# Optimization experiments

Measured on AMD Instinct MI355X. Metric: run time of the kernel, lower is better.

Reference implementation:

```python
import jax, jax.numpy as jnp
import numpy as np

B, DX, DY, H, T, L = 256, 256, 256, 512, 128, 2
EPS = 1e-5


def setup_inputs() -> dict:
    key = jax.random.key(0)
    ks = jax.random.split(key, 16)
    s = 0.02
    return {
        "inputx": jax.random.normal(ks[0], (B, DX, T), dtype=jnp.float32),
        "inputy": jax.random.normal(ks[1], (B, DY, T), dtype=jnp.float32),
        # stacked gate weights: f,i,o for T-path and F-path, [L, 3H, Dx+Dy+H]
        "WTg": jax.random.normal(ks[2], (L, 3 * H, DX + DY + H), dtype=jnp.float32) * s,
        "bTg": jax.random.normal(ks[3], (L, 3 * H), dtype=jnp.float32) * s,
        "WFg": jax.random.normal(ks[4], (L, 3 * H, DX + DY + H), dtype=jnp.float32) * s,
        "bFg": jax.random.normal(ks[5], (L, 3 * H), dtype=jnp.float32) * s,
        # candidate cell weights
        "WTc": jax.random.normal(ks[6], (L, H, DX + H), dtype=jnp.float32) * s,
        "bTc": jax.random.normal(ks[7], (L, H), dtype=jnp.float32) * s,
        "WFc": jax.random.normal(ks[8], (L, H, DY + H), dtype=jnp.float32) * s,
        "bFc": jax.random.normal(ks[9], (L, H), dtype=jnp.float32) * s,
        # batchnorm affine params per layer
        "gammaT": jnp.ones((L, H), dtype=jnp.float32),
        "betaT": jnp.zeros((L, H), dtype=jnp.float32),
        "gammaF": jnp.ones((L, H), dtype=jnp.float32),
        "betaF": jnp.zeros((L, H), dtype=jnp.float32),
    }


def _batchnorm(h, gamma, beta):
    # train-mode BN over batch dim, biased variance (torch semantics)
    mu = jnp.mean(h, axis=0, keepdims=True)
    var = jnp.mean((h - mu) ** 2, axis=0, keepdims=True)
    return (h - mu) * jax.lax.rsqrt(var + EPS) * gamma + beta


def _forward(inputx, inputy, WTg, bTg, WFg, bFg, WTc, bTc, WFc, bFc,
             gammaT, betaT, gammaF, betaF):
    nL = WTg.shape[0]
    b, h = inputx.shape[0], gammaT.shape[1]
    zeros = jnp.zeros((nL, b, h), dtype=inputx.dtype)

    def step(carry, xy):
        hT, hF, CT, CF = carry  # each [L, B, H]
        x, y = xy  # [B, Dx], [B, Dy]
        hT_n, hF_n, CT_n, CF_n = [], [], [], []
        for i in range(nL):
            catT = jnp.concatenate([x, y, hT[i]], axis=1)
            catF = jnp.concatenate([x, y, hF[i]], axis=1)
            gT = jax.nn.sigmoid(catT @ WTg[i].T + bTg[i])  # [B, 3H]
            gF = jax.nn.sigmoid(catF @ WFg[i].T + bFg[i])
            fT, iT, oT = jnp.split(gT, 3, axis=1)
            fF, iF, oF = jnp.split(gF, 3, axis=1)
            cT = jnp.tanh(jnp.concatenate([x, hT[i]], axis=1) @ WTc[i].T + bTc[i])
            cF = jnp.tanh(jnp.concatenate([y, hF[i]], axis=1) @ WFc[i].T + bFc[i])
            CTi = fT * CT[i] + iT * cT
            CFi = fF * CF[i] + iF * cF
            hTi = oT * jnp.tanh(CTi)
            hFi = oF * jnp.tanh(CFi)
            hT_n.append(hTi); hF_n.append(hFi); CT_n.append(CTi); CF_n.append(CFi)
        hT = jnp.stack(hT_n); hF = jnp.stack(hF_n)
        CT = jnp.stack(CT_n); CF = jnp.stack(CF_n)
        # output comes from last layer only; BN in train mode
        outT = _batchnorm(hT[-1], gammaT[-1], betaT[-1])
        outF = _batchnorm(hF[-1], gammaF[-1], betaF[-1])
        return (hT, hF, CT, CF), (outT, outF)

    xs = (jnp.transpose(inputx, (2, 0, 1)), jnp.transpose(inputy, (2, 0, 1)))
    _, (outT_seq, outF_seq) = jax.lax.scan(step, (zeros, zeros, zeros, zeros), xs)
    # [T, B, H] -> [B, H, T] (torch.stack(..., dim=2))
    return jnp.transpose(outT_seq, (1, 2, 0)), jnp.transpose(outF_seq, (1, 2, 0))


def reference(inputx, inputy, WTg, bTg, WFg, bFg, WTc, bTc, WFc, bFc,
              gammaT, betaT, gammaF, betaF):
    return _forward(inputx, inputy, WTg, bTg, WFg, bFg, WTc, bTc, WFc, bFc,
                    gammaT, betaT, gammaF, betaF)
```

## Files before the change

### kernel.cpp

```cpp
#include <hip/hip_runtime.h>

#define NBLK 256
#define NTHR 512

typedef __attribute__((ext_vector_type(8))) short s16x8;
typedef __attribute__((ext_vector_type(8))) __bf16 bf16x8;
typedef __attribute__((ext_vector_type(4))) float f32x4;

__device__ __forceinline__ ushort f2bf(float f) {
  uint u = __float_as_uint(f);
  return (ushort)((u + 0x7FFFu + ((u >> 16) & 1u)) >> 16);
}
__device__ __forceinline__ float bf2f(ushort s) {
  return __uint_as_float(((uint)s) << 16);
}
__device__ __forceinline__ float sigm(float x) { return 1.f / (1.f + __expf(-x)); }
__device__ __forceinline__ float tanhf_(float x) {
  x = fminf(9.f, fmaxf(-9.f, x));
  float e = __expf(2.f * x);
  return (e - 1.f) / (e + 1.f);
}

__global__ void init_k(uint* __restrict__ bar) {
  int i = blockIdx.x * blockDim.x + threadIdx.x;
  if (i < 512) bar[i] = 0u;
}

__global__ void xyt_k(const float* __restrict__ x, const float* __restrict__ y,
                      ushort* __restrict__ xyT) {
  __shared__ ushort sT[64 * 130];
  const int bid = blockIdx.x;
  const int chunk = bid & 7;
  const int b = bid >> 3;
  const int d0 = (chunk & 3) * 64;
  const float* src = ((chunk < 4) ? x : y) + ((size_t)b * 256 + d0) * 128;
  const int tid = threadIdx.x;
  const int tt = tid & 127, rr = tid >> 7;
#pragma unroll
  for (int i = 0; i < 32; ++i) {
    int row = i * 2 + rr;
    sT[row * 130 + tt] = f2bf(src[(size_t)row * 128 + tt]);
  }
  __syncthreads();
  const int dbase = ((chunk < 4) ? 0 : 256) + d0;
#pragma unroll
  for (int i = 0; i < 16; ++i) {
    int idx = tid + i * 256;
    int t = idx >> 5, j = idx & 31;
    uint v = (uint)sT[(2 * j) * 130 + t] | ((uint)sT[(2 * j + 1) * 130 + t] << 16);
    *(uint*)(xyT + ((size_t)t * 256 + b) * 512 + dbase + 2 * j) = v;
  }
}

__launch_bounds__(NTHR, 2)
__global__ void seq_k(const ushort* __restrict__ xyT,
                      ushort* __restrict__ hist,
                      const float* __restrict__ WTg, const float* __restrict__ WFg,
                      const float* __restrict__ WTc, const float* __restrict__ WFc,
                      const float* __restrict__ bTg, const float* __restrict__ bFg,
                      const float* __restrict__ bTc, const float* __restrict__ bFc,
                      uint* bar) {
  extern __shared__ char smem[];
  float* sAcc = (float*)(smem + 98304);

  const int tid = threadIdx.x;
  const int bid = blockIdx.x;
  const int mt = bid & 7;
  const int cg = (bid >> 3) & 15;
  const int s = bid >> 7;
  const int g = s * 8 + mt;
  const int m0 = mt * 32;
  const int j0 = cg * 32;
  const int w = tid >> 6;
  const int l = tid & 63;
  const int l15 = l & 15;
  const int q16 = (l >> 4) * 16;
  const bool isGate = (w < 6);
  uint* fl = bar + (g << 4);

  s16x8 wreg[32];
  if (isGate) {
    const int gt = w >> 1, half = w & 1;
    const float* Wp = ((s == 0) ? WTg : WFg) + 1572864
                    + ((size_t)(gt * 512 + j0 + half * 16 + l15)) * 1024 + (q16 >> 1);
#pragma unroll
    for (int kk = 0; kk < 32; ++kk) {
      s16x8 v;
#pragma unroll
      for (int e = 0; e < 8; ++e) v[e] = (short)f2bf(Wp[kk * 32 + e]);
      wreg[kk] = v;
    }
  } else {
    const int half = w & 1;
    const float* Wp = ((s == 0) ? WTc : WFc) + 393216
                    + ((size_t)(j0 + half * 16 + l15)) * 768 + (q16 >> 1);
#pragma unroll
    for (int kk = 0; kk < 24; ++kk) {
      s16x8 v;
#pragma unroll
      for (int e = 0; e < 8; ++e) v[e] = (short)f2bf(Wp[kk * 32 + e]);
      wreg[kk] = v;
    }
  }

  const int ro = tid >> 4;
  const int cc0 = (tid & 15) * 2;
  const int ehalf = cc0 >> 4;
  const int ec16 = cc0 & 15;
  float bfv0, bfv1, biv0, biv1, bov0, bov1, bcv0, bcv1;
  {
    const float* bg = ((s == 0) ? bTg : bFg) + 1536;
    const float* bc = ((s == 0) ? bTc : bFc) + 512;
    int col = j0 + cc0;
    bfv0 = bg[col];        bfv1 = bg[col + 1];
    biv0 = bg[512 + col];  biv1 = bg[513 + col];
    bov0 = bg[1024 + col]; bov1 = bg[1025 + col];
    bcv0 = bc[col];        bcv1 = bc[col + 1];
  }
  float C0 = 0.f, C1 = 0.f;

  auto stage_row = [&](const ushort* gbase, char* lbase, int r) {
    const char* srow = (const char*)(gbase + (size_t)r * 512);
    int off = (l * 16) ^ ((r & 7) << 4);
    __builtin_amdgcn_global_load_lds(
        (const __attribute__((address_space(1))) void*)(srow + off),
        (__attribute__((address_space(3))) void*)(lbase + (r << 10)), 16, 0, 0);
  };
  auto stage_row_coh = [&](const ushort* gbase, char* lbase, int r) {
    const char* srow = (const char*)(gbase + (size_t)r * 512);
    int off = (l * 16) ^ ((r & 7) << 4);
    __builtin_amdgcn_global_load_lds(
        (const __attribute__((address_space(1))) void*)(srow + off),
        (__attribute__((address_space(3))) void*)(lbase + (r << 10)), 16, 0, 17);
  };

  {
#pragma unroll
    for (int i = 0; i < 4; ++i) stage_row(xyT + (size_t)m0 * 512, smem, (w << 2) + i);
  }
  __syncthreads();

  const int sw = (l15 & 7) << 4;
  for (int t = 0; t < 128; ++t) {
    const int cur = t & 1;
    char* xyb = smem + cur * 32768;
    char* xybn = smem + (cur ^ 1) * 32768;
    char* hb = smem + 65536;

    f32x4 acc0 = {0.f, 0.f, 0.f, 0.f};
    f32x4 acc1 = {0.f, 0.f, 0.f, 0.f};

    {
      const char* base0 = xyb + (l15 << 10);
      const char* base1 = xyb + ((16 + l15) << 10);
      if (isGate) {
#pragma unroll
        for (int kk = 0; kk < 16; ++kk) {
          int c2 = (kk * 64 + q16) ^ sw;
          s16x8 a0 = *(const s16x8*)(base0 + c2);
          s16x8 a1 = *(const s16x8*)(base1 + c2);
          acc0 = __builtin_amdgcn_mfma_f32_16x16x32_bf16(
              __builtin_bit_cast(bf16x8, a0), __builtin_bit_cast(bf16x8, wreg[kk]), acc0, 0, 0, 0);
          acc1 = __builtin_amdgcn_mfma_f32_16x16x32_bf16(
              __builtin_bit_cast(bf16x8, a1), __builtin_bit_cast(bf16x8, wreg[kk]), acc1, 0, 0, 0);
        }
      } else {
#pragma unroll
        for (int kk = 0; kk < 8; ++kk) {
          int c2 = ((s * 512 + kk * 64 + q16)) ^ sw;
          s16x8 a0 = *(const s16x8*)(base0 + c2);
          s16x8 a1 = *(const s16x8*)(base1 + c2);
          acc0 = __builtin_amdgcn_mfma_f32_16x16x32_bf16(
              __builtin_bit_cast(bf16x8, a0), __builtin_bit_cast(bf16x8, wreg[kk]), acc0, 0, 0, 0);
          acc1 = __builtin_amdgcn_mfma_f32_16x16x32_bf16(
              __builtin_bit_cast(bf16x8, a1), __builtin_bit_cast(bf16x8, wreg[kk]), acc1, 0, 0, 0);
        }
      }
    }

    if (w == 0 && t) {
      const uint tgt = (uint)t;
      while (true) {
        uint v = (l < 16)
                     ? __hip_atomic_load(fl + l, __ATOMIC_RELAXED, __HIP_MEMORY_SCOPE_SYSTEM)
                     : tgt;
        if (__all((int)(v >= tgt))) break;
        __builtin_amdgcn_s_sleep(1);
      }
    }
    __builtin_amdgcn_s_barrier();

    if (t) {
      const ushort* hsrc = hist + (((size_t)s * 128 + (t - 1)) * 256 + m0) * 512;
#pragma unroll
      for (int i = 0; i < 4; ++i) stage_row_coh(hsrc, hb, (w << 2) + i);
    }
    {
      const int tn = (t < 127) ? t + 1 : 127;
      const ushort* xyNext = xyT + ((size_t)(tn * 256 + m0)) * 512;
#pragma unroll
      for (int i = 0; i < 4; ++i) stage_row(xyNext, xybn, (w << 2) + i);
    }

    asm volatile("s_waitcnt vmcnt(4)" ::: "memory");
    __builtin_amdgcn_sched_barrier(0);
    __builtin_amdgcn_s_barrier();
    __builtin_amdgcn_sched_barrier(0);

    if (t) {
      const char* base0 = hb + (l15 << 10);
      const char* base1 = hb + ((16 + l15) << 10);
      if (isGate) {
#pragma unroll
        for (int kk = 0; kk < 16; ++kk) {
          int c2 = (kk * 64 + q16) ^ sw;
          s16x8 a0 = *(const s16x8*)(base0 + c2);
          s16x8 a1 = *(const s16x8*)(base1 + c2);
          acc0 = __builtin_amdgcn_mfma_f32_16x16x32_bf16(
              __builtin_bit_cast(bf16x8, a0), __builtin_bit_cast(bf16x8, wreg[16 + kk]), acc0, 0, 0, 0);
          acc1 = __builtin_amdgcn_mfma_f32_16x16x32_bf16(
              __builtin_bit_cast(bf16x8, a1), __builtin_bit_cast(bf16x8, wreg[16 + kk]), acc1, 0, 0, 0);
        }
      } else {
#pragma unroll
        for (int kk = 0; kk < 16; ++kk) {
          int c2 = (kk * 64 + q16) ^ sw;
          s16x8 a0 = *(const s16x8*)(base0 + c2);
          s16x8 a1 = *(const s16x8*)(base1 + c2);
          acc0 = __builtin_amdgcn_mfma_f32_16x16x32_bf16(
              __builtin_bit_cast(bf16x8, a0), __builtin_bit_cast(bf16x8, wreg[8 + kk]), acc0, 0, 0, 0);
          acc1 = __builtin_amdgcn_mfma_f32_16x16x32_bf16(
              __builtin_bit_cast(bf16x8, a1), __builtin_bit_cast(bf16x8, wreg[8 + kk]), acc1, 0, 0, 0);
        }
      }
    }

#pragma unroll
    for (int rg = 0; rg < 4; ++rg) {
      sAcc[w * 576 + ((q16 >> 2) + rg) * 18 + l15] = acc0[rg];
      sAcc[w * 576 + (16 + (q16 >> 2) + rg) * 18 + l15] = acc1[rg];
    }
    asm volatile("s_waitcnt lgkmcnt(0)" ::: "memory");
    __builtin_amdgcn_sched_barrier(0);
    __builtin_amdgcn_s_barrier();
    __builtin_amdgcn_sched_barrier(0);

    {
      const float2 pf = *(const float2*)&sAcc[(0 + ehalf) * 576 + ro * 18 + ec16];
      const float2 pi = *(const float2*)&sAcc[(2 + ehalf) * 576 + ro * 18 + ec16];
      const float2 po = *(const float2*)&sAcc[(4 + ehalf) * 576 + ro * 18 + ec16];
      const float2 pc = *(const float2*)&sAcc[(6 + ehalf) * 576 + ro * 18 + ec16];
      float f0 = sigm(pf.x + bfv0), f1 = sigm(pf.y + bfv1);
      float i0 = sigm(pi.x + biv0), i1 = sigm(pi.y + biv1);
      float o0 = sigm(po.x + bov0), o1 = sigm(po.y + bov1);
      float c0 = tanhf_(pc.x + bcv0), c1 = tanhf_(pc.y + bcv1);
      C0 = f0 * C0 + i0 * c0;
      C1 = f1 * C1 + i1 * c1;
      float h0 = o0 * tanhf_(C0);
      float h1 = o1 * tanhf_(C1);
      uint hp = (uint)f2bf(h0) | (((uint)f2bf(h1)) << 16);
      __hip_atomic_store(
          (uint*)(hist + (((size_t)s * 128 + t) * 256 + m0 + ro) * 512 + j0 + cc0), hp,
          __ATOMIC_RELAXED, __HIP_MEMORY_SCOPE_SYSTEM);
    }
    __syncthreads();
    if (tid == 0)
      __hip_atomic_store(fl + cg, (uint)(t + 1), __ATOMIC_RELAXED, __HIP_MEMORY_SCOPE_SYSTEM);
  }
}

__global__ void bnstat_k(const ushort* __restrict__ hist,
                         const float* __restrict__ gT, const float* __restrict__ beT,
                         const float* __restrict__ gF, const float* __restrict__ beF,
                         float* __restrict__ scale, float* __restrict__ shift) {
  const int t = blockIdx.x >> 1, s = blockIdx.x & 1;
  const int tid = threadIdx.x;
  const ushort* hp = hist + ((size_t)s * 128 + t) * 256 * 512;
  const float* gp = (s ? gF : gT) + 512;
  const float* bp = (s ? beF : beT) + 512;
#pragma unroll
  for (int hh = 0; hh < 2; ++hh) {
    const int h = tid + hh * 256;
    float sum = 0.f, sq = 0.f;
#pragma unroll 8
    for (int b = 0; b < 256; ++b) {
      float v = bf2f(hp[(size_t)b * 512 + h]);
      sum += v;
      sq += v * v;
    }
    float mu = sum * 0.00390625f;
    float var = sq * 0.00390625f - mu * mu;
    float sc = (1.0f / sqrtf(var + 1e-5f)) * gp[h];
    size_t o = ((size_t)s * 128 + t) * 512 + h;
    scale[o] = sc;
    shift[o] = bp[h] - mu * sc;
  }
}

__global__ void bnwrite_k(const ushort* __restrict__ hist, const float* __restrict__ scale,
                          const float* __restrict__ shift, float* __restrict__ out) {
  __shared__ float sT[64 * 129];
  const int bid = blockIdx.x;
  const int hc = bid & 7, b = (bid >> 3) & 255, s = bid >> 11;
  const int h0 = hc * 64;
  const int tid = threadIdx.x;
  const int hh = tid & 63, tq = tid >> 6;
#pragma unroll 4
  for (int tc = 0; tc < 32; ++tc) {
    const int t = tc * 4 + tq;
    const size_t so = ((size_t)s * 128 + t) * 512 + h0 + hh;
    float v = bf2f(hist[(((size_t)s * 128 + t) * 256 + b) * 512 + h0 + hh]);
    sT[hh * 129 + t] = v * scale[so] + shift[so];
  }
  __syncthreads();
  const int t2 = tid & 127, hq = tid >> 7;
#pragma unroll 4
  for (int i = 0; i < 32; ++i) {
    const int h = i * 2 + hq;
    out[(size_t)s * 16777216 + ((size_t)b * 512 + h0 + h) * 128 + t2] = sT[h * 129 + t2];
  }
}

extern "C" void kernel_launch(void* const* d_in, const int* in_sizes, int n_in,
                              void* d_out, int out_size, void* d_ws, size_t ws_size,
                              hipStream_t stream) {
  const float* inputx = (const float*)d_in[0];
  const float* inputy = (const float*)d_in[1];
  const float* WTg = (const float*)d_in[2];
  const float* bTg = (const float*)d_in[3];
  const float* WFg = (const float*)d_in[4];
  const float* bFg = (const float*)d_in[5];
  const float* WTc = (const float*)d_in[6];
  const float* bTc = (const float*)d_in[7];
  const float* WFc = (const float*)d_in[8];
  const float* bFc = (const float*)d_in[9];
  const float* gT = (const float*)d_in[10];
  const float* beT = (const float*)d_in[11];
  const float* gF = (const float*)d_in[12];
  const float* beF = (const float*)d_in[13];
  float* out = (float*)d_out;

  char* ws = (char*)d_ws;
  ushort* xyT = (ushort*)ws;
  ushort* hist = (ushort*)(ws + 34603008);
  float* scale = (float*)(ws + 101711872);
  float* shift = (float*)(ws + 102236160);
  uint* bar = (uint*)(ws + 102760448);

  init_k<<<2, 256, 0, stream>>>(bar);
  xyt_k<<<2048, 256, 0, stream>>>(inputx, inputy, xyT);

  hipFuncSetAttribute((const void*)seq_k, hipFuncAttributeMaxDynamicSharedMemorySize, 116736);
  void* args[11];
  args[0] = &xyT; args[1] = &hist;
  args[2] = &WTg; args[3] = &WFg; args[4] = &WTc; args[5] = &WFc;
  args[6] = &bTg; args[7] = &bFg; args[8] = &bTc; args[9] = &bFc;
  args[10] = &bar;
  hipLaunchCooperativeKernel((const void*)seq_k, dim3(NBLK), dim3(NTHR), args, 116736, stream);

  bnstat_k<<<256, 256, 0, stream>>>(hist, gT, beT, gF, beF, scale, shift);
  bnwrite_k<<<4096, 256, 0, stream>>>(hist, scale, shift, out);
}
```

Before: 611.6 us.

## Split wave work along K instead of N to reuse A fragments across two MFMA tiles

Each wave now covers both 16-column halves of its gate and half of the K range, rather than one column half over the full K range. Every A fragment read from LDS feeds two MFMAs, which halves the LDS read traffic per MFMA. The two K-partial sums are written to a wider shared accumulator and added during the elementwise gate stage. This adds LDS capacity for the accumulators, four accumulators per wave, and an extra add per gate element.

```diff
diff --git a/kernel.cpp b/kernel.cpp
--- a/kernel.cpp
+++ b/kernel.cpp
@@ -20,6 +20,9 @@
   float e = __expf(2.f * x);
   return (e - 1.f) / (e + 1.f);
 }
+
+#define MFMA(a, b, c) __builtin_amdgcn_mfma_f32_16x16x32_bf16( \
+    __builtin_bit_cast(bf16x8, a), __builtin_bit_cast(bf16x8, b), c, 0, 0, 0)
 
 __global__ void init_k(uint* __restrict__ bar) {
   int i = blockIdx.x * blockDim.x + threadIdx.x;
@@ -76,37 +79,55 @@
   const int l15 = l & 15;
   const int q16 = (l >> 4) * 16;
   const bool isGate = (w < 6);
+  const int kh = w & 1;
   uint* fl = bar + (g << 4);
 
-  s16x8 wreg[32];
+  s16x8 wreg[2][16];
   if (isGate) {
-    const int gt = w >> 1, half = w & 1;
-    const float* Wp = ((s == 0) ? WTg : WFg) + 1572864
-                    + ((size_t)(gt * 512 + j0 + half * 16 + l15)) * 1024 + (q16 >> 1);
-#pragma unroll
-    for (int kk = 0; kk < 32; ++kk) {
-      s16x8 v;
-#pragma unroll
-      for (int e = 0; e < 8; ++e) v[e] = (short)f2bf(Wp[kk * 32 + e]);
-      wreg[kk] = v;
+    const int gt = w >> 1;
+#pragma unroll
+    for (int p = 0; p < 2; ++p) {
+      const float* Wrow = ((s == 0) ? WTg : WFg) + 1572864
+                        + ((size_t)(gt * 512 + j0 + p * 16 + l15)) * 1024 + (q16 >> 1);
+#pragma unroll
+      for (int kk = 0; kk < 8; ++kk) {
+        s16x8 v;
+#pragma unroll
+        for (int e = 0; e < 8; ++e) v[e] = (short)f2bf(Wrow[kh * 256 + kk * 32 + e]);
+        wreg[p][kk] = v;
+      }
+#pragma unroll
+      for (int kk = 0; kk < 8; ++kk) {
+        s16x8 v;
+#pragma unroll
+        for (int e = 0; e < 8; ++e) v[e] = (short)f2bf(Wrow[512 + kh * 256 + kk * 32 + e]);
+        wreg[p][8 + kk] = v;
+      }
     }
   } else {
-    const int half = w & 1;
-    const float* Wp = ((s == 0) ? WTc : WFc) + 393216
-                    + ((size_t)(j0 + half * 16 + l15)) * 768 + (q16 >> 1);
-#pragma unroll
-    for (int kk = 0; kk < 24; ++kk) {
-      s16x8 v;
-#pragma unroll
-      for (int e = 0; e < 8; ++e) v[e] = (short)f2bf(Wp[kk * 32 + e]);
-      wreg[kk] = v;
+#pragma unroll
+    for (int p = 0; p < 2; ++p) {
+      const float* Wrow = ((s == 0) ? WTc : WFc) + 393216
+                        + ((size_t)(j0 + p * 16 + l15)) * 768 + (q16 >> 1);
+#pragma unroll
+      for (int kk = 0; kk < 4; ++kk) {
+        s16x8 v;
+#pragma unroll
+        for (int e = 0; e < 8; ++e) v[e] = (short)f2bf(Wrow[kh * 128 + kk * 32 + e]);
+        wreg[p][kk] = v;
+      }
+#pragma unroll
+      for (int kk = 0; kk < 8; ++kk) {
+        s16x8 v;
+#pragma unroll
+        for (int e = 0; e < 8; ++e) v[e] = (short)f2bf(Wrow[256 + kh * 256 + kk * 32 + e]);
+        wreg[p][4 + kk] = v;
+      }
     }
   }
 
   const int ro = tid >> 4;
   const int cc0 = (tid & 15) * 2;
-  const int ehalf = cc0 >> 4;
-  const int ec16 = cc0 & 15;
   float bfv0, bfv1, biv0, biv1, bov0, bov1, bcv0, bcv1;
   {
     const float* bg = ((s == 0) ? bTg : bFg) + 1536;
@@ -147,33 +168,35 @@
     char* xybn = smem + (cur ^ 1) * 32768;
     char* hb = smem + 65536;
 
-    f32x4 acc0 = {0.f, 0.f, 0.f, 0.f};
-    f32x4 acc1 = {0.f, 0.f, 0.f, 0.f};
+    f32x4 acc00 = {0.f, 0.f, 0.f, 0.f};
+    f32x4 acc01 = {0.f, 0.f, 0.f, 0.f};
+    f32x4 acc10 = {0.f, 0.f, 0.f, 0.f};
+    f32x4 acc11 = {0.f, 0.f, 0.f, 0.f};
 
     {
       const char* base0 = xyb + (l15 << 10);
       const char* base1 = xyb + ((16 + l15) << 10);
       if (isGate) {
 #pragma unroll
-        for (int kk = 0; kk < 16; ++kk) {
-          int c2 = (kk * 64 + q16) ^ sw;
+        for (int kk = 0; kk < 8; ++kk) {
+          int c2 = (kh * 512 + kk * 64 + q16) ^ sw;
           s16x8 a0 = *(const s16x8*)(base0 + c2);
           s16x8 a1 = *(const s16x8*)(base1 + c2);
-          acc0 = __builtin_amdgcn_mfma_f32_16x16x32_bf16(
-              __builtin_bit_cast(bf16x8, a0), __builtin_bit_cast(bf16x8, wreg[kk]), acc0, 0, 0, 0);
-          acc1 = __builtin_amdgcn_mfma_f32_16x16x32_bf16(
-              __builtin_bit_cast(bf16x8, a1), __builtin_bit_cast(bf16x8, wreg[kk]), acc1, 0, 0, 0);
+          acc00 = MFMA(a0, wreg[0][kk], acc00);
+          acc01 = MFMA(a1, wreg[0][kk], acc01);
+          acc10 = MFMA(a0, wreg[1][kk], acc10);
+          acc11 = MFMA(a1, wreg[1][kk], acc11);
         }
       } else {
 #pragma unroll
-        for (int kk = 0; kk < 8; ++kk) {
-          int c2 = ((s * 512 + kk * 64 + q16)) ^ sw;
+        for (int kk = 0; kk < 4; ++kk) {
+          int c2 = (s * 512 + kh * 256 + kk * 64 + q16) ^ sw;
           s16x8 a0 = *(const s16x8*)(base0 + c2);
           s16x8 a1 = *(const s16x8*)(base1 + c2);
-          acc0 = __builtin_amdgcn_mfma_f32_16x16x32_bf16(
-              __builtin_bit_cast(bf16x8, a0), __builtin_bit_cast(bf16x8, wreg[kk]), acc0, 0, 0, 0);
-          acc1 = __builtin_amdgcn_mfma_f32_16x16x32_bf16(
-              __builtin_bit_cast(bf16x8, a1), __builtin_bit_cast(bf16x8, wreg[kk]), acc1, 0, 0, 0);
+          acc00 = MFMA(a0, wreg[0][kk], acc00);
+          acc01 = MFMA(a1, wreg[0][kk], acc01);
+          acc10 = MFMA(a0, wreg[1][kk], acc10);
+          acc11 = MFMA(a1, wreg[1][kk], acc11);
         }
       }
     }
@@ -212,33 +235,39 @@
       const char* base1 = hb + ((16 + l15) << 10);
       if (isGate) {
 #pragma unroll
-        for (int kk = 0; kk < 16; ++kk) {
-          int c2 = (kk * 64 + q16) ^ sw;
+        for (int kk = 0; kk < 8; ++kk) {
+          int c2 = (kh * 512 + kk * 64 + q16) ^ sw;
           s16x8 a0 = *(const s16x8*)(base0 + c2);
           s16x8 a1 = *(const s16x8*)(base1 + c2);
-          acc0 = __builtin_amdgcn_mfma_f32_16x16x32_bf16(
-              __builtin_bit_cast(bf16x8, a0), __builtin_bit_cast(bf16x8, wreg[16 + kk]), acc0, 0, 0, 0);
-          acc1 = __builtin_amdgcn_mfma_f32_16x16x32_bf16(
-              __builtin_bit_cast(bf16x8, a1), __builtin_bit_cast(bf16x8, wreg[16 + kk]), acc1, 0, 0, 0);
+          acc00 = MFMA(a0, wreg[0][8 + kk], acc00);
+          acc01 = MFMA(a1, wreg[0][8 + kk], acc01);
+          acc10 = MFMA(a0, wreg[1][8 + kk], acc10);
+          acc11 = MFMA(a1, wreg[1][8 + kk], acc11);
         }
       } else {
 #pragma unroll
-        for (int kk = 0; kk < 16; ++kk) {
-          int c2 = (kk * 64 + q16) ^ sw;
+        for (int kk = 0; kk < 8; ++kk) {
+          int c2 = (kh * 512 + kk * 64 + q16) ^ sw;
           s16x8 a0 = *(const s16x8*)(base0 + c2);
           s16x8 a1 = *(const s16x8*)(base1 + c2);
-          acc0 = __builtin_amdgcn_mfma_f32_16x16x32_bf16(
-              __builtin_bit_cast(bf16x8, a0), __builtin_bit_cast(bf16x8, wreg[8 + kk]), acc0, 0, 0, 0);
-          acc1 = __builtin_amdgcn_mfma_f32_16x16x32_bf16(
-              __builtin_bit_cast(bf16x8, a1), __builtin_bit_cast(bf16x8, wreg[8 + kk]), acc1, 0, 0, 0);
+          acc00 = MFMA(a0, wreg[0][4 + kk], acc00);
+          acc01 = MFMA(a1, wreg[0][4 + kk], acc01);
+          acc10 = MFMA(a0, wreg[1][4 + kk], acc10);
+          acc11 = MFMA(a1, wreg[1][4 + kk], acc11);
         }
       }
     }
 
-#pragma unroll
-    for (int rg = 0; rg < 4; ++rg) {
-      sAcc[w * 576 + ((q16 >> 2) + rg) * 18 + l15] = acc0[rg];
-      sAcc[w * 576 + (16 + (q16 >> 2) + rg) * 18 + l15] = acc1[rg];
+    {
+      float* sl = sAcc + w * 1088 + l15;
+      const int r0 = q16 >> 2;
+#pragma unroll
+      for (int rg = 0; rg < 4; ++rg) {
+        sl[(r0 + rg) * 34] = acc00[rg];
+        sl[(16 + r0 + rg) * 34] = acc01[rg];
+        sl[(r0 + rg) * 34 + 16] = acc10[rg];
+        sl[(16 + r0 + rg) * 34 + 16] = acc11[rg];
+      }
     }
     asm volatile("s_waitcnt lgkmcnt(0)" ::: "memory");
     __builtin_amdgcn_sched_barrier(0);
@@ -246,14 +275,19 @@
     __builtin_amdgcn_sched_barrier(0);
 
     {
-      const float2 pf = *(const float2*)&sAcc[(0 + ehalf) * 576 + ro * 18 + ec16];
-      const float2 pi = *(const float2*)&sAcc[(2 + ehalf) * 576 + ro * 18 + ec16];
-      const float2 po = *(const float2*)&sAcc[(4 + ehalf) * 576 + ro * 18 + ec16];
-      const float2 pc = *(const float2*)&sAcc[(6 + ehalf) * 576 + ro * 18 + ec16];
-      float f0 = sigm(pf.x + bfv0), f1 = sigm(pf.y + bfv1);
-      float i0 = sigm(pi.x + biv0), i1 = sigm(pi.y + biv1);
-      float o0 = sigm(po.x + bov0), o1 = sigm(po.y + bov1);
-      float c0 = tanhf_(pc.x + bcv0), c1 = tanhf_(pc.y + bcv1);
+      const int eb = ro * 34 + cc0;
+      float2 f0v = *(const float2*)&sAcc[eb];
+      float2 f1v = *(const float2*)&sAcc[1088 + eb];
+      float2 i0v = *(const float2*)&sAcc[2176 + eb];
+      float2 i1v = *(const float2*)&sAcc[3264 + eb];
+      float2 o0v = *(const float2*)&sAcc[4352 + eb];
+      float2 o1v = *(const float2*)&sAcc[5440 + eb];
+      float2 c0v = *(const float2*)&sAcc[6528 + eb];
+      float2 c1v = *(const float2*)&sAcc[7616 + eb];
+      float f0 = sigm(f0v.x + f1v.x + bfv0), f1 = sigm(f0v.y + f1v.y + bfv1);
+      float i0 = sigm(i0v.x + i1v.x + biv0), i1 = sigm(i0v.y + i1v.y + biv1);
+      float o0 = sigm(o0v.x + o1v.x + bov0), o1 = sigm(o0v.y + o1v.y + bov1);
+      float c0 = tanhf_(c0v.x + c1v.x + bcv0), c1 = tanhf_(c0v.y + c1v.y + bcv1);
       C0 = f0 * C0 + i0 * c0;
       C1 = f1 * C1 + i1 * c1;
       float h0 = o0 * tanhf_(C0);
@@ -350,13 +384,13 @@
   init_k<<<2, 256, 0, stream>>>(bar);
   xyt_k<<<2048, 256, 0, stream>>>(inputx, inputy, xyT);
 
-  hipFuncSetAttribute((const void*)seq_k, hipFuncAttributeMaxDynamicSharedMemorySize, 116736);
+  hipFuncSetAttribute((const void*)seq_k, hipFuncAttributeMaxDynamicSharedMemorySize, 133120);
   void* args[11];
   args[0] = &xyT; args[1] = &hist;
   args[2] = &WTg; args[3] = &WFg; args[4] = &WTc; args[5] = &WFc;
   args[6] = &bTg; args[7] = &bFg; args[8] = &bTc; args[9] = &bFc;
   args[10] = &bar;
-  hipLaunchCooperativeKernel((const void*)seq_k, dim3(NBLK), dim3(NTHR), args, 116736, stream);
+  hipLaunchCooperativeKernel((const void*)seq_k, dim3(NBLK), dim3(NTHR), args, 133120, stream);
 
   bnstat_k<<<256, 256, 0, stream>>>(hist, gT, beT, gF, beF, scale, shift);
   bnwrite_k<<<4096, 256, 0, stream>>>(hist, scale, shift, out);
```

Result: faster. 545.7 us (median of 3 runs) (-10.8%).
